# Kernel tuning notes

Measured on AMD Instinct MI355X. Metric: run time of the kernel, lower is better.

## Reference

```python
import jax, jax.numpy as jnp
import numpy as np

B, S, C, H = 8, 1024, 768, 8
D = C // H  # head dim = 96
MLP = 4 * C


def setup_inputs() -> dict:
    key = jax.random.key(0)
    ks = jax.random.split(key, 12)
    sc = 0.02
    return {
        "x": jax.random.normal(ks[0], (B, S, C), jnp.float32),
        "ln1_w": jnp.ones((S, C), jnp.float32),
        "ln1_b": jnp.zeros((S, C), jnp.float32),
        "ln2_w": jnp.ones((S, C), jnp.float32),
        "ln2_b": jnp.zeros((S, C), jnp.float32),
        "qkv_w": jax.random.normal(ks[1], (C, 3 * C), jnp.float32) * sc,
        "proj_w": jax.random.normal(ks[2], (C, C), jnp.float32) * sc,
        "mlp_w1": jax.random.normal(ks[3], (C, MLP), jnp.float32) * sc,
        "mlp_b1": jnp.zeros((MLP,), jnp.float32),
        "mlp_w2": jax.random.normal(ks[4], (MLP, C), jnp.float32) * sc,
        "mlp_b2": jnp.zeros((C,), jnp.float32),
    }


def _layernorm2d(x, w, b, eps=1e-5):
    # normalizes over BOTH (seq, channel) dims, per nn.LayerNorm([length, channel])
    mu = jnp.mean(x, axis=(-2, -1), keepdims=True)
    var = jnp.mean(jnp.square(x - mu), axis=(-2, -1), keepdims=True)
    return (x - mu) * jax.lax.rsqrt(var + eps) * w + b


def _attention(x, qkv_w, proj_w):
    b, s, _ = x.shape
    qkv = (x @ qkv_w).reshape(b, s, 3, H, D)
    q, k, v = qkv[:, :, 0], qkv[:, :, 1], qkv[:, :, 2]  # [b, s, h, d]
    # NOTE: original module applies NO 1/sqrt(d) scaling
    scores = jnp.einsum("bshd,bthd->bhst", q, k)
    attn = jax.nn.softmax(scores, axis=-1)
    out = jnp.einsum("bhst,bthd->bshd", attn, v).reshape(b, s, C)
    return out @ proj_w


def reference(x, ln1_w, ln1_b, ln2_w, ln2_b, qkv_w, proj_w, mlp_w1, mlp_b1, mlp_w2, mlp_b2):
    # dropout is identity in eval mode
    h = x + _attention(_layernorm2d(x, ln1_w, ln1_b), qkv_w, proj_w)
    y = _layernorm2d(h, ln2_w, ln2_b)
    y = jax.nn.gelu(y @ mlp_w1 + mlp_b1, approximate=False)
    return h + (y @ mlp_w2 + mlp_b2)
```

## Files before the change

kernel.cpp:

```cpp
#include <hip/hip_runtime.h>
#include <hip/hip_bf16.h>

#define S_LEN 1024
#define NB 8
#define NC 768
#define NH 8
#define HD 96
#define NMLP 3072
#define SC (S_LEN*NC)
#define BS (NB*S_LEN)

typedef __attribute__((ext_vector_type(8))) unsigned short u16x8;
typedef __attribute__((ext_vector_type(4))) unsigned short u16x4;
typedef __attribute__((ext_vector_type(8))) __bf16 bf16x8;
typedef __attribute__((ext_vector_type(4))) float f32x4;

__device__ __forceinline__ unsigned short f2b(float f) {
  union { __hip_bfloat16 h; unsigned short u; } cvt;
  cvt.h = __float2bfloat16(f);
  return cvt.u;
}

__device__ __forceinline__ void gload16(const unsigned short* g, unsigned short* l) {
  __builtin_amdgcn_global_load_lds(
      (const __attribute__((address_space(1))) unsigned int*)g,
      (__attribute__((address_space(3))) unsigned int*)l, 16, 0, 0);
}

__device__ __forceinline__ float gelu_f(float v) {
  float u = v * (0.7978845608f + 0.0356774081f * v * v);
  float au = fabsf(u);
  float e = __expf(-2.0f * au);
  float th = (1.0f - e) / (1.0f + e);
  th = copysignf(th, u);
  return 0.5f * v * (1.0f + th);
}

template<int EPI>
__global__ __launch_bounds__(512, 1)
void gemm8(const unsigned short* __restrict__ A, int lda,
           const unsigned short* __restrict__ Bt, int ldb,
           void* __restrict__ Cv, int ldc, int K,
           const float* __restrict__ bias,
           const float* __restrict__ residual, int ldr)
{
  __shared__ unsigned short As[3*16384];
  __shared__ unsigned short Bs[3*8192];
  const int tid = threadIdx.x, lane = tid & 63, wid = tid >> 6;
  const int wm = wid & 3, wn = wid >> 2;
  const int r15 = lane & 15, g = lane >> 4;
  const int tm = blockIdx.x * 256, tn = blockIdx.y * 128;
  const int NT = K >> 6;

  const int srow = lane >> 3;
  const int scol = ((lane & 7) ^ srow) << 3;
  const unsigned short* Ag = A  + (size_t)(tm + wid*32 + srow)*lda + scol;
  const unsigned short* Bg = Bt + (size_t)(tn + wid*16 + srow)*ldb + scol;

  const int kx  = (r15 & 7) << 4;
  const int k0b = (g*16) ^ kx;
  const int k1b = (64 + g*16) ^ kx;
  char* AsB = (char*)As;
  char* BsB = (char*)Bs;
  const int arow = (wm*64 + r15) * 128;
  const int brow = (wn*64 + r15) * 128;

#define LDA8(m,ks) (*(const bf16x8*)(AsB + bufA + arow + (m)*2048 + ((ks) ? k1b : k0b)))
#define LDB8(n,ks) (*(const bf16x8*)(BsB + bufB + brow + (n)*2048 + ((ks) ? k1b : k0b)))
#define STGA(i,kk,bf) gload16(Ag + (size_t)((i)*8)*lda + (kk), As + (bf)*16384 + (wid*4 + (i))*512)
#define STGB(i,kk,bf) gload16(Bg + (size_t)((i)*8)*ldb + (kk), Bs + (bf)*8192  + (wid*2 + (i))*512)
#define MFMA16(a8,b8,c) __builtin_amdgcn_mfma_f32_16x16x32_bf16(a8, b8, c, 0, 0, 0)

  f32x4 acc[4][4];
  #pragma unroll
  for (int m = 0; m < 4; ++m)
    #pragma unroll
    for (int n = 0; n < 4; ++n)
      acc[m][n] = (f32x4){0.f, 0.f, 0.f, 0.f};

  STGA(0,0,0); STGA(1,0,0); STGA(2,0,0); STGA(3,0,0); STGB(0,0,0); STGB(1,0,0);
  STGA(0,64,1); STGA(1,64,1); STGA(2,64,1); STGA(3,64,1); STGB(0,64,1); STGB(1,64,1);
  asm volatile("s_waitcnt vmcnt(6)" ::: "memory");
  __builtin_amdgcn_s_barrier();

  int buf = 0, nbuf = 2;
  for (int t = 0; t < NT; ++t) {
    const int kk = (t + 2) << 6;
    const bool pre = (t + 2) < NT;
    const int bufA = buf * 32768;
    const int bufB = buf * 16384;
    bf16x8 a[4][2], b0[2][2], b1[2][2];

    #pragma unroll
    for (int m = 0; m < 4; ++m) { a[m][0] = LDA8(m,0); a[m][1] = LDA8(m,1); }
    #pragma unroll
    for (int n = 0; n < 2; ++n) { b0[n][0] = LDB8(n,0); b0[n][1] = LDB8(n,1); }
    if (pre) { STGA(0,kk,nbuf); STGA(1,kk,nbuf); STGB(0,kk,nbuf); }
    __builtin_amdgcn_s_barrier();
    asm volatile("s_waitcnt lgkmcnt(0)" ::: "memory");
    __builtin_amdgcn_s_setprio(1);
    #pragma unroll
    for (int m = 0; m < 4; ++m)
      #pragma unroll
      for (int n = 0; n < 2; ++n) {
        acc[m][n] = MFMA16(a[m][0], b0[n][0], acc[m][n]);
        acc[m][n] = MFMA16(a[m][1], b0[n][1], acc[m][n]);
      }
    __builtin_amdgcn_s_setprio(0);
    __builtin_amdgcn_s_barrier();

    #pragma unroll
    for (int n = 0; n < 2; ++n) { b1[n][0] = LDB8(n+2,0); b1[n][1] = LDB8(n+2,1); }
    if (pre) { STGA(2,kk,nbuf); STGA(3,kk,nbuf); STGB(1,kk,nbuf); }
    __builtin_amdgcn_s_barrier();
    asm volatile("s_waitcnt lgkmcnt(0)" ::: "memory");
    __builtin_amdgcn_s_setprio(1);
    #pragma unroll
    for (int m = 0; m < 4; ++m)
      #pragma unroll
      for (int n = 0; n < 2; ++n) {
        acc[m][n+2] = MFMA16(a[m][0], b1[n][0], acc[m][n+2]);
        acc[m][n+2] = MFMA16(a[m][1], b1[n][1], acc[m][n+2]);
      }
    __builtin_amdgcn_s_setprio(0);
    if (pre) asm volatile("s_waitcnt vmcnt(6)" ::: "memory");
    else     asm volatile("s_waitcnt vmcnt(0)" ::: "memory");
    __builtin_amdgcn_s_barrier();
    buf  = (buf  == 2) ? 0 : buf  + 1;
    nbuf = (nbuf == 2) ? 0 : nbuf + 1;
  }
#undef LDA8
#undef LDB8
#undef STGA
#undef STGB
#undef MFMA16

  unsigned short* Cu = (unsigned short*)Cv;
  float* Cf = (float*)Cv;
  #pragma unroll
  for (int m = 0; m < 4; ++m) {
    #pragma unroll
    for (int n = 0; n < 4; ++n) {
      const int col = tn + wn*64 + n*16 + r15;
      #pragma unroll
      for (int r = 0; r < 4; ++r) {
        const int row = tm + wm*64 + m*16 + g*4 + r;
        float v = acc[m][n][r];
        if (EPI == 2 || EPI == 4) v += bias[col];
        if (EPI == 3 || EPI == 4) v += residual[(size_t)row*ldr + col];
        if (EPI == 2) v = gelu_f(v);
        if (EPI == 0 || EPI == 2) Cu[(size_t)row*ldc + col] = f2b(v);
        else                      Cf[(size_t)row*ldc + col] = v;
      }
    }
  }
}

__global__ __launch_bounds__(256, 2)
void flash_attn(const unsigned short* __restrict__ qkv,
                const unsigned short* __restrict__ vt,
                unsigned short* __restrict__ outb)
{
  __shared__ unsigned short Ks[128*96];
  __shared__ unsigned short Vs[96*128];
  __shared__ unsigned short Ps[128*128];
  const int tid = threadIdx.x, lane = tid & 63, wq = tid >> 6;
  const int r15 = lane & 15, g = lane >> 4;
  const int bh = blockIdx.y, b = bh >> 3, h = bh & 7;
  const int q0 = blockIdx.x * 128;
  const int swz = (r15 & 7) << 4;
  char* PsB = (char*)Ps;
  char* VsB = (char*)Vs;

  bf16x8 qf[2][3];
  {
    const unsigned short* qb = qkv + ((size_t)b*S_LEN + q0 + wq*32 + r15)*2304 + h*HD + g*8;
    #pragma unroll
    for (int n = 0; n < 2; ++n)
      #pragma unroll
      for (int kc = 0; kc < 3; ++kc)
        qf[n][kc] = *(const bf16x8*)(qb + (size_t)n*16*2304 + kc*32);
  }

  int krow[6], kcol[6], vrow[6], vcol[6];
  #pragma unroll
  for (int i = 0; i < 6; ++i) {
    const int c = (wq*6 + i)*64 + lane;
    krow[i] = c / 12;
    kcol[i] = (c % 12) * 8;
    const int L = c * 16;
    const int row = L >> 8, cb = L & 255;
    vrow[i] = row;
    vcol[i] = (cb ^ ((row & 7) << 4)) >> 1;
  }
  const unsigned short* kbase = qkv + (size_t)b*S_LEN*2304 + NC + h*HD;
  const unsigned short* vbase = vt + (size_t)bh*HD*S_LEN;

  f32x4 oacc[6][2];
  #pragma unroll
  for (int m = 0; m < 6; ++m) {
    oacc[m][0] = (f32x4){0.f,0.f,0.f,0.f};
    oacc[m][1] = (f32x4){0.f,0.f,0.f,0.f};
  }
  float mrun[2] = {-INFINITY, -INFINITY};
  float lrun[2] = {0.f, 0.f};

  for (int kt = 0; kt < 8; ++kt) {
    const unsigned short* ksrc = kbase + (size_t)kt*128*2304;
    const unsigned short* vsrc = vbase + kt*128;
    #pragma unroll
    for (int i = 0; i < 6; ++i) {
      gload16(ksrc + (size_t)krow[i]*2304 + kcol[i], Ks + (wq*6 + i)*512);
      gload16(vsrc + vrow[i]*1024 + vcol[i],         Vs + (wq*6 + i)*512);
    }
    __syncthreads();

    f32x4 sacc[8][2];
    #pragma unroll
    for (int m = 0; m < 8; ++m) {
      sacc[m][0] = (f32x4){0.f,0.f,0.f,0.f};
      sacc[m][1] = (f32x4){0.f,0.f,0.f,0.f};
    }
    __builtin_amdgcn_s_setprio(1);
    #pragma unroll
    for (int kc = 0; kc < 3; ++kc)
      #pragma unroll
      for (int m = 0; m < 8; ++m) {
        bf16x8 kf = *(const bf16x8*)(Ks + (m*16 + r15)*96 + kc*32 + g*8);
        sacc[m][0] = __builtin_amdgcn_mfma_f32_16x16x32_bf16(kf, qf[0][kc], sacc[m][0], 0,0,0);
        sacc[m][1] = __builtin_amdgcn_mfma_f32_16x16x32_bf16(kf, qf[1][kc], sacc[m][1], 0,0,0);
      }
    __builtin_amdgcn_s_setprio(0);

    #pragma unroll
    for (int n = 0; n < 2; ++n) {
      float pm = -INFINITY;
      #pragma unroll
      for (int m = 0; m < 8; ++m)
        #pragma unroll
        for (int r = 0; r < 4; ++r) pm = fmaxf(pm, sacc[m][n][r]);
      pm = fmaxf(pm, __shfl_xor(pm, 16));
      pm = fmaxf(pm, __shfl_xor(pm, 32));
      const float newm = fmaxf(mrun[n], pm);
      const float scale = __expf(mrun[n] - newm);
      mrun[n] = newm;
      const int qloc = wq*32 + n*16 + r15;
      float s = 0.f;
      #pragma unroll
      for (int m = 0; m < 8; ++m) {
        float e0 = __expf(sacc[m][n][0] - newm);
        float e1 = __expf(sacc[m][n][1] - newm);
        float e2 = __expf(sacc[m][n][2] - newm);
        float e3 = __expf(sacc[m][n][3] - newm);
        s += (e0 + e1) + (e2 + e3);
        u16x4 pk = { f2b(e0), f2b(e1), f2b(e2), f2b(e3) };
        *(u16x4*)(PsB + ((qloc*256 + m*32 + g*8) ^ swz)) = pk;
      }
      s += __shfl_xor(s, 16);
      s += __shfl_xor(s, 32);
      lrun[n] = lrun[n]*scale + s;
      #pragma unroll
      for (int m = 0; m < 6; ++m) oacc[m][n] *= scale;
    }

    #pragma unroll
    for (int kc = 0; kc < 4; ++kc) {
      bf16x8 pf0 = *(const bf16x8*)(PsB + (((wq*32      + r15)*256 + kc*64 + g*16) ^ swz));
      bf16x8 pf1 = *(const bf16x8*)(PsB + (((wq*32 + 16 + r15)*256 + kc*64 + g*16) ^ swz));
      __builtin_amdgcn_s_setprio(1);
      #pragma unroll
      for (int m = 0; m < 6; ++m) {
        bf16x8 vf = *(const bf16x8*)(VsB + (((m*16 + r15)*256 + kc*64 + g*16) ^ swz));
        oacc[m][0] = __builtin_amdgcn_mfma_f32_16x16x32_bf16(vf, pf0, oacc[m][0], 0,0,0);
        oacc[m][1] = __builtin_amdgcn_mfma_f32_16x16x32_bf16(vf, pf1, oacc[m][1], 0,0,0);
      }
      __builtin_amdgcn_s_setprio(0);
    }
    __syncthreads();
  }

  #pragma unroll
  for (int n = 0; n < 2; ++n) {
    const float inv = 1.0f / lrun[n];
    unsigned short* orow = outb + ((size_t)b*S_LEN + q0 + wq*32 + n*16 + r15)*NC + h*HD;
    #pragma unroll
    for (int m = 0; m < 6; ++m) {
      u16x4 pk = { f2b(oacc[m][n][0]*inv), f2b(oacc[m][n][1]*inv),
                   f2b(oacc[m][n][2]*inv), f2b(oacc[m][n][3]*inv) };
      *(u16x4*)(orow + m*16 + g*4) = pk;
    }
  }
}

__global__ void transpose_cast(const float* __restrict__ W, unsigned short* __restrict__ Wt,
                               int K, int N)
{
  __shared__ float tile[32][33];
  const int tx = threadIdx.x & 31, ty = threadIdx.x >> 5;
  const int n0 = blockIdx.x * 32, k0 = blockIdx.y * 32;
  #pragma unroll
  for (int i = 0; i < 32; i += 8)
    tile[ty + i][tx] = W[(size_t)(k0 + ty + i)*N + n0 + tx];
  __syncthreads();
  #pragma unroll
  for (int i = 0; i < 32; i += 8)
    Wt[(size_t)(n0 + ty + i)*K + k0 + tx] = f2b(tile[tx][ty + i]);
}

__global__ void transpose_v(const unsigned short* __restrict__ qkv, unsigned short* __restrict__ vt)
{
  __shared__ unsigned short tile[32][33];
  const int bh = blockIdx.z, b = bh >> 3, h = bh & 7;
  const unsigned short* v = qkv + (size_t)b*S_LEN*3*NC + 2*NC + h*HD;
  unsigned short* o = vt + (size_t)bh*HD*S_LEN;
  const int s0 = blockIdx.x * 32, d0 = blockIdx.y * 32;
  const int tx = threadIdx.x & 31, ty = threadIdx.x >> 5;
  #pragma unroll
  for (int i = 0; i < 32; i += 8)
    tile[ty + i][tx] = v[(size_t)(s0 + ty + i)*(3*NC) + d0 + tx];
  __syncthreads();
  #pragma unroll
  for (int i = 0; i < 32; i += 8)
    o[(size_t)(d0 + ty + i)*S_LEN + s0 + tx] = tile[tx][ty + i];
}

__global__ void ln_part(const float* __restrict__ X, float* __restrict__ part)
{
  const int b = blockIdx.x / 96, blk = blockIdx.x % 96;
  const float4* xb = (const float4*)(X + (size_t)b*SC);
  float s = 0.f, s2 = 0.f;
  #pragma unroll
  for (int i = 0; i < 8; ++i) {
    float4 v = xb[blk*2048 + i*256 + threadIdx.x];
    s  += v.x + v.y + v.z + v.w;
    s2 += v.x*v.x + v.y*v.y + v.z*v.z + v.w*v.w;
  }
  #pragma unroll
  for (int o = 32; o; o >>= 1) { s += __shfl_down(s, o); s2 += __shfl_down(s2, o); }
  __shared__ float r1[4], r2[4];
  const int w = threadIdx.x >> 6;
  if ((threadIdx.x & 63) == 0) { r1[w] = s; r2[w] = s2; }
  __syncthreads();
  if (threadIdx.x == 0) {
    part[(b*96 + blk)*2]     = r1[0] + r1[1] + r1[2] + r1[3];
    part[(b*96 + blk)*2 + 1] = r2[0] + r2[1] + r2[2] + r2[3];
  }
}

__global__ void ln_fin(const float* __restrict__ part, float* __restrict__ stats)
{
  const int b = blockIdx.x;
  float s = 0.f, s2 = 0.f;
  for (int i = threadIdx.x; i < 96; i += 64) {
    s  += part[(b*96 + i)*2];
    s2 += part[(b*96 + i)*2 + 1];
  }
  #pragma unroll
  for (int o = 32; o; o >>= 1) { s += __shfl_down(s, o); s2 += __shfl_down(s2, o); }
  if (threadIdx.x == 0) {
    const float inv = 1.0f / (float)SC;
    const float mu = s * inv;
    const float var = s2 * inv - mu*mu;
    stats[b*2] = mu;
    stats[b*2 + 1] = rsqrtf(var + 1e-5f);
  }
}

__global__ void ln_apply(const float* __restrict__ X, const float* __restrict__ W,
                         const float* __restrict__ Bv, const float* __restrict__ stats,
                         unsigned short* __restrict__ out)
{
  const size_t i = ((size_t)blockIdx.x*256 + threadIdx.x) * 8;
  const int b = (int)(i / SC);
  const size_t r = i % SC;
  const float mu = stats[b*2], rs = stats[b*2 + 1];
  float4 x0 = *(const float4*)(X + i),  x1 = *(const float4*)(X + i + 4);
  float4 w0 = *(const float4*)(W + r),  w1 = *(const float4*)(W + r + 4);
  float4 b0 = *(const float4*)(Bv + r), b1 = *(const float4*)(Bv + r + 4);
  u16x8 o;
  o[0] = f2b((x0.x - mu)*rs*w0.x + b0.x);
  o[1] = f2b((x0.y - mu)*rs*w0.y + b0.y);
  o[2] = f2b((x0.z - mu)*rs*w0.z + b0.z);
  o[3] = f2b((x0.w - mu)*rs*w0.w + b0.w);
  o[4] = f2b((x1.x - mu)*rs*w1.x + b1.x);
  o[5] = f2b((x1.y - mu)*rs*w1.y + b1.y);
  o[6] = f2b((x1.z - mu)*rs*w1.z + b1.z);
  o[7] = f2b((x1.w - mu)*rs*w1.w + b1.w);
  *(u16x8*)(out + i) = o;
}

extern "C" void kernel_launch(void* const* d_in, const int* in_sizes, int n_in,
                              void* d_out, int out_size, void* d_ws, size_t ws_size,
                              hipStream_t stream) {
  const float* x      = (const float*)d_in[0];
  const float* ln1_w  = (const float*)d_in[1];
  const float* ln1_b  = (const float*)d_in[2];
  const float* ln2_w  = (const float*)d_in[3];
  const float* ln2_b  = (const float*)d_in[4];
  const float* qkv_w  = (const float*)d_in[5];
  const float* proj_w = (const float*)d_in[6];
  const float* mlp_w1 = (const float*)d_in[7];
  const float* mlp_b1 = (const float*)d_in[8];
  const float* mlp_w2 = (const float*)d_in[9];
  const float* mlp_b2 = (const float*)d_in[10];
  float* out = (float*)d_out;

  char* ws = (char*)d_ws;
  size_t off = 0;
  auto alloc = [&](size_t b) { size_t o = off; off += (b + 255) & ~(size_t)255; return o; };
  unsigned short* wqkvT  = (unsigned short*)(ws + alloc((size_t)3*NC*NC*2));
  unsigned short* wprojT = (unsigned short*)(ws + alloc((size_t)NC*NC*2));
  unsigned short* w1T    = (unsigned short*)(ws + alloc((size_t)NMLP*NC*2));
  unsigned short* w2T    = (unsigned short*)(ws + alloc((size_t)NC*NMLP*2));
  unsigned short* lnbf   = (unsigned short*)(ws + alloc((size_t)BS*NC*2));
  const size_t qkvOff    = alloc((size_t)BS*3*NC*2);
  unsigned short* qkvbf  = (unsigned short*)(ws + qkvOff);
  unsigned short* vt     = (unsigned short*)(ws + alloc((size_t)NB*NH*HD*S_LEN*2));
  unsigned short* ybf    = (unsigned short*)(ws + qkvOff);
  float* hbuf            = (float*)(ws + alloc((size_t)BS*NC*4));
  float* part            = (float*)(ws + alloc((size_t)NB*96*2*4));
  float* stats           = (float*)(ws + alloc((size_t)NB*2*4));
  (void)ws_size; (void)in_sizes; (void)n_in; (void)out_size;

  const dim3 blk(256);
  const dim3 blk512(512);

  transpose_cast<<<dim3(3*NC/32, NC/32),   blk, 0, stream>>>(qkv_w,  wqkvT,  NC, 3*NC);
  transpose_cast<<<dim3(NC/32, NC/32),     blk, 0, stream>>>(proj_w, wprojT, NC, NC);
  transpose_cast<<<dim3(NMLP/32, NC/32),   blk, 0, stream>>>(mlp_w1, w1T,    NC, NMLP);
  transpose_cast<<<dim3(NC/32, NMLP/32),   blk, 0, stream>>>(mlp_w2, w2T,    NMLP, NC);

  ln_part<<<dim3(NB*96), blk, 0, stream>>>(x, part);
  ln_fin<<<dim3(NB), dim3(64), 0, stream>>>(part, stats);
  ln_apply<<<dim3(BS*NC/2048), blk, 0, stream>>>(x, ln1_w, ln1_b, stats, lnbf);

  gemm8<0><<<dim3(BS/256, 3*NC/128), blk512, 0, stream>>>(
      lnbf, NC, wqkvT, NC, qkvbf, 3*NC, NC, nullptr, nullptr, 0);

  transpose_v<<<dim3(S_LEN/32, HD/32, NB*NH), blk, 0, stream>>>(qkvbf, vt);

  flash_attn<<<dim3(S_LEN/128, NB*NH), blk, 0, stream>>>(qkvbf, vt, lnbf);

  gemm8<3><<<dim3(BS/256, NC/128), blk512, 0, stream>>>(
      lnbf, NC, wprojT, NC, hbuf, NC, NC, nullptr, x, NC);

  ln_part<<<dim3(NB*96), blk, 0, stream>>>(hbuf, part);
  ln_fin<<<dim3(NB), dim3(64), 0, stream>>>(part, stats);
  ln_apply<<<dim3(BS*NC/2048), blk, 0, stream>>>(hbuf, ln2_w, ln2_b, stats, lnbf);

  gemm8<2><<<dim3(BS/256, NMLP/128), blk512, 0, stream>>>(
      lnbf, NC, w1T, NC, ybf, NMLP, NC, mlp_b1, nullptr, 0);

  gemm8<4><<<dim3(BS/256, NC/128), blk512, 0, stream>>>(
      ybf, NMLP, w2T, NMLP, out, NC, NMLP, mlp_b2, hbuf, NC);
}
```

Before: 283.6 us.

## Fuse LN2 statistics into proj GEMM epilogue and add 256x256 MLP1 GEMM

The projection GEMM epilogue now accumulates per-batch sum and sum-of-squares and adds them atomically into a small buffer. This removes the separate ln_part/ln_fin passes over hbuf, and a new ln_apply_f computes mean and variance from those sums. A new 256x256-tile GEMM with double-buffered LDS replaces the 256x128 kernel for the MLP up-projection to raise data reuse per block. The single-pass E[x^2]-mu^2 variance in fp32 risks cancellation error. The atomics also make the statistics order-dependent from run to run.

```diff
diff --git a/kernel.cpp b/kernel.cpp
--- a/kernel.cpp
+++ b/kernel.cpp
@@ -38,11 +38,152 @@
 
 template<int EPI>
 __global__ __launch_bounds__(512, 1)
+void gemm256(const unsigned short* __restrict__ A, int lda,
+             const unsigned short* __restrict__ Bt, int ldb,
+             void* __restrict__ Cv, int ldc, int K,
+             const float* __restrict__ bias,
+             const float* __restrict__ residual, int ldr)
+{
+  __shared__ unsigned short As[4*8192];
+  __shared__ unsigned short Bs[4*8192];
+  const int tid = threadIdx.x, lane = tid & 63, wid = tid >> 6;
+  const int wm = wid & 1, wn = wid >> 1;
+  const int r15 = lane & 15, g = lane >> 4;
+  const int tm = blockIdx.x * 256, tn = blockIdx.y * 256;
+  const int NT = K >> 6;
+
+  const int srow = lane >> 3;
+  const int schunk = ((lane & 7) ^ srow) << 3;
+  const unsigned short* Ag = A  + (size_t)(tm + wid*16 + srow)*lda + schunk;
+  const unsigned short* Bg = Bt + (size_t)(tn + wid*16 + srow)*ldb + schunk;
+
+  const int c0 = ((g)     ^ (r15 & 7)) << 4;
+  const int c1 = ((4 | g) ^ (r15 & 7)) << 4;
+  char* AsB = (char*)As;
+  char* BsB = (char*)Bs;
+
+#define STGA(h,i,kk,sl) gload16(Ag + (size_t)((h)*128 + (i)*8)*lda + (kk), As + (sl)*8192 + (wid*16 + (i)*8)*64)
+#define STGB(h,i,kk,sl) gload16(Bg + (size_t)((h)*128 + (i)*8)*ldb + (kk), Bs + (sl)*8192 + (wid*16 + (i)*8)*64)
+#define LDA8(fm,cb,sl) (*(const bf16x8*)(AsB + (sl)*16384 + ((fm)*16 + r15)*128 + (cb)))
+#define LDB8(n,cb,sl)  (*(const bf16x8*)(BsB + (sl)*16384 + ((wn&1)*64 + (n)*16 + r15)*128 + (cb)))
+#define MFMA(a8,b8,c) __builtin_amdgcn_mfma_f32_16x16x32_bf16(a8, b8, c, 0, 0, 0)
+
+  f32x4 acc[8][4];
+  #pragma unroll
+  for (int m = 0; m < 8; ++m)
+    #pragma unroll
+    for (int n = 0; n < 4; ++n)
+      acc[m][n] = (f32x4){0.f, 0.f, 0.f, 0.f};
+
+  STGA(0,0,0,0); STGA(0,1,0,0); STGA(1,0,0,1); STGA(1,1,0,1);
+  STGB(0,0,0,0); STGB(0,1,0,0); STGB(1,0,0,1); STGB(1,1,0,1);
+  asm volatile("s_waitcnt vmcnt(0)" ::: "memory");
+  __builtin_amdgcn_s_barrier();
+
+  for (int kt = 0; kt < NT; ++kt) {
+    const int rd = (kt & 1) * 2, wr = rd ^ 2;
+    const int kk = (kt + 1) << 6;
+    const bool pre = (kt + 1) < NT;
+    const int asl = rd + wm;
+    const int bsl = rd + (wn >> 1);
+    bf16x8 a[4], b[4];
+
+    #pragma unroll
+    for (int m = 0; m < 4; ++m) a[m] = LDA8(m, c0, asl);
+    #pragma unroll
+    for (int n = 0; n < 4; ++n) b[n] = LDB8(n, c0, bsl);
+    if (pre) { STGA(0,0,kk,wr); STGA(0,1,kk,wr); }
+    __builtin_amdgcn_s_barrier();
+    asm volatile("s_waitcnt lgkmcnt(0)" ::: "memory");
+    __builtin_amdgcn_s_setprio(1);
+    #pragma unroll
+    for (int m = 0; m < 4; ++m)
+      #pragma unroll
+      for (int n = 0; n < 4; ++n)
+        acc[m][n] = MFMA(a[m], b[n], acc[m][n]);
+    __builtin_amdgcn_s_setprio(0);
+    __builtin_amdgcn_s_barrier();
+
+    #pragma unroll
+    for (int m = 0; m < 4; ++m) a[m] = LDA8(m + 4, c0, asl);
+    if (pre) { STGA(1,0,kk,wr+1); STGA(1,1,kk,wr+1); }
+    __builtin_amdgcn_s_barrier();
+    asm volatile("s_waitcnt lgkmcnt(0)" ::: "memory");
+    __builtin_amdgcn_s_setprio(1);
+    #pragma unroll
+    for (int m = 0; m < 4; ++m)
+      #pragma unroll
+      for (int n = 0; n < 4; ++n)
+        acc[m + 4][n] = MFMA(a[m], b[n], acc[m + 4][n]);
+    __builtin_amdgcn_s_setprio(0);
+    __builtin_amdgcn_s_barrier();
+
+    #pragma unroll
+    for (int m = 0; m < 4; ++m) a[m] = LDA8(m, c1, asl);
+    #pragma unroll
+    for (int n = 0; n < 4; ++n) b[n] = LDB8(n, c1, bsl);
+    if (pre) { STGB(0,0,kk,wr); STGB(0,1,kk,wr); }
+    __builtin_amdgcn_s_barrier();
+    asm volatile("s_waitcnt lgkmcnt(0)" ::: "memory");
+    __builtin_amdgcn_s_setprio(1);
+    #pragma unroll
+    for (int m = 0; m < 4; ++m)
+      #pragma unroll
+      for (int n = 0; n < 4; ++n)
+        acc[m][n] = MFMA(a[m], b[n], acc[m][n]);
+    __builtin_amdgcn_s_setprio(0);
+    __builtin_amdgcn_s_barrier();
+
+    #pragma unroll
+    for (int m = 0; m < 4; ++m) a[m] = LDA8(m + 4, c1, asl);
+    if (pre) { STGB(1,0,kk,wr+1); STGB(1,1,kk,wr+1); }
+    __builtin_amdgcn_s_barrier();
+    asm volatile("s_waitcnt lgkmcnt(0)" ::: "memory");
+    __builtin_amdgcn_s_setprio(1);
+    #pragma unroll
+    for (int m = 0; m < 4; ++m)
+      #pragma unroll
+      for (int n = 0; n < 4; ++n)
+        acc[m + 4][n] = MFMA(a[m], b[n], acc[m + 4][n]);
+    __builtin_amdgcn_s_setprio(0);
+    asm volatile("s_waitcnt vmcnt(0)" ::: "memory");
+    __builtin_amdgcn_s_barrier();
+  }
+#undef STGA
+#undef STGB
+#undef LDA8
+#undef LDB8
+#undef MFMA
+
+  unsigned short* Cu = (unsigned short*)Cv;
+  float* Cf = (float*)Cv;
+  #pragma unroll
+  for (int m = 0; m < 8; ++m) {
+    #pragma unroll
+    for (int n = 0; n < 4; ++n) {
+      const int col = tn + wn*64 + n*16 + r15;
+      #pragma unroll
+      for (int r = 0; r < 4; ++r) {
+        const int row = tm + wm*128 + m*16 + g*4 + r;
+        float v = acc[m][n][r];
+        if (EPI == 2 || EPI == 4) v += bias[col];
+        if (EPI == 3 || EPI == 4) v += residual[(size_t)row*ldr + col];
+        if (EPI == 2) v = gelu_f(v);
+        if (EPI == 0 || EPI == 2) Cu[(size_t)row*ldc + col] = f2b(v);
+        else                      Cf[(size_t)row*ldc + col] = v;
+      }
+    }
+  }
+}
+
+template<int EPI>
+__global__ __launch_bounds__(512, 1)
 void gemm8(const unsigned short* __restrict__ A, int lda,
            const unsigned short* __restrict__ Bt, int ldb,
            void* __restrict__ Cv, int ldc, int K,
            const float* __restrict__ bias,
-           const float* __restrict__ residual, int ldr)
+           const float* __restrict__ residual, int ldr,
+           float* __restrict__ lnred)
 {
   __shared__ unsigned short As[3*16384];
   __shared__ unsigned short Bs[3*8192];
@@ -137,6 +278,7 @@
 
   unsigned short* Cu = (unsigned short*)Cv;
   float* Cf = (float*)Cv;
+  float s1 = 0.f, s2 = 0.f;
   #pragma unroll
   for (int m = 0; m < 4; ++m) {
     #pragma unroll
@@ -149,9 +291,26 @@
         if (EPI == 2 || EPI == 4) v += bias[col];
         if (EPI == 3 || EPI == 4) v += residual[(size_t)row*ldr + col];
         if (EPI == 2) v = gelu_f(v);
+        if (EPI == 3) { s1 += v; s2 += v*v; }
         if (EPI == 0 || EPI == 2) Cu[(size_t)row*ldc + col] = f2b(v);
         else                      Cf[(size_t)row*ldc + col] = v;
       }
+    }
+  }
+  if (EPI == 3) {
+    #pragma unroll
+    for (int o = 32; o; o >>= 1) { s1 += __shfl_xor(s1, o); s2 += __shfl_xor(s2, o); }
+    __syncthreads();
+    float* red = (float*)As;
+    if (lane == 0) { red[wid*2] = s1; red[wid*2+1] = s2; }
+    __syncthreads();
+    if (tid == 0) {
+      float a1 = 0.f, a2 = 0.f;
+      #pragma unroll
+      for (int w = 0; w < 8; ++w) { a1 += red[w*2]; a2 += red[w*2+1]; }
+      const int bidx = tm >> 10;
+      atomicAdd(&lnred[bidx*2],     a1);
+      atomicAdd(&lnred[bidx*2 + 1], a2);
     }
   }
 }
@@ -389,6 +548,32 @@
   *(u16x8*)(out + i) = o;
 }
 
+__global__ void ln_apply_f(const float* __restrict__ X, const float* __restrict__ W,
+                           const float* __restrict__ Bv, const float* __restrict__ red,
+                           unsigned short* __restrict__ out)
+{
+  const size_t i = ((size_t)blockIdx.x*256 + threadIdx.x) * 8;
+  const int b = (int)(i / SC);
+  const size_t r = i % SC;
+  const float inv = 1.0f / (float)SC;
+  const float mu = red[b*2] * inv;
+  const float var = red[b*2 + 1] * inv - mu*mu;
+  const float rs = rsqrtf(var + 1e-5f);
+  float4 x0 = *(const float4*)(X + i),  x1 = *(const float4*)(X + i + 4);
+  float4 w0 = *(const float4*)(W + r),  w1 = *(const float4*)(W + r + 4);
+  float4 b0 = *(const float4*)(Bv + r), b1 = *(const float4*)(Bv + r + 4);
+  u16x8 o;
+  o[0] = f2b((x0.x - mu)*rs*w0.x + b0.x);
+  o[1] = f2b((x0.y - mu)*rs*w0.y + b0.y);
+  o[2] = f2b((x0.z - mu)*rs*w0.z + b0.z);
+  o[3] = f2b((x0.w - mu)*rs*w0.w + b0.w);
+  o[4] = f2b((x1.x - mu)*rs*w1.x + b1.x);
+  o[5] = f2b((x1.y - mu)*rs*w1.y + b1.y);
+  o[6] = f2b((x1.z - mu)*rs*w1.z + b1.z);
+  o[7] = f2b((x1.w - mu)*rs*w1.w + b1.w);
+  *(u16x8*)(out + i) = o;
+}
+
 extern "C" void kernel_launch(void* const* d_in, const int* in_sizes, int n_in,
                               void* d_out, int out_size, void* d_ws, size_t ws_size,
                               hipStream_t stream) {
@@ -420,10 +605,13 @@
   float* hbuf            = (float*)(ws + alloc((size_t)BS*NC*4));
   float* part            = (float*)(ws + alloc((size_t)NB*96*2*4));
   float* stats           = (float*)(ws + alloc((size_t)NB*2*4));
+  float* lnred           = (float*)(ws + alloc((size_t)NB*2*4));
   (void)ws_size; (void)in_sizes; (void)n_in; (void)out_size;
 
   const dim3 blk(256);
   const dim3 blk512(512);
+
+  hipMemsetAsync(lnred, 0, NB*2*sizeof(float), stream);
 
   transpose_cast<<<dim3(3*NC/32, NC/32),   blk, 0, stream>>>(qkv_w,  wqkvT,  NC, 3*NC);
   transpose_cast<<<dim3(NC/32, NC/32),     blk, 0, stream>>>(proj_w, wprojT, NC, NC);
@@ -435,22 +623,20 @@
   ln_apply<<<dim3(BS*NC/2048), blk, 0, stream>>>(x, ln1_w, ln1_b, stats, lnbf);
 
   gemm8<0><<<dim3(BS/256, 3*NC/128), blk512, 0, stream>>>(
-      lnbf, NC, wqkvT, NC, qkvbf, 3*NC, NC, nullptr, nullptr, 0);
+      lnbf, NC, wqkvT, NC, qkvbf, 3*NC, NC, nullptr, nullptr, 0, nullptr);
 
   transpose_v<<<dim3(S_LEN/32, HD/32, NB*NH), blk, 0, stream>>>(qkvbf, vt);
 
   flash_attn<<<dim3(S_LEN/128, NB*NH), blk, 0, stream>>>(qkvbf, vt, lnbf);
 
   gemm8<3><<<dim3(BS/256, NC/128), blk512, 0, stream>>>(
-      lnbf, NC, wprojT, NC, hbuf, NC, NC, nullptr, x, NC);
-
-  ln_part<<<dim3(NB*96), blk, 0, stream>>>(hbuf, part);
-  ln_fin<<<dim3(NB), dim3(64), 0, stream>>>(part, stats);
-  ln_apply<<<dim3(BS*NC/2048), blk, 0, stream>>>(hbuf, ln2_w, ln2_b, stats, lnbf);
-
-  gemm8<2><<<dim3(BS/256, NMLP/128), blk512, 0, stream>>>(
+      lnbf, NC, wprojT, NC, hbuf, NC, NC, nullptr, x, NC, lnred);
+
+  ln_apply_f<<<dim3(BS*NC/2048), blk, 0, stream>>>(hbuf, ln2_w, ln2_b, lnred, lnbf);
+
+  gemm256<2><<<dim3(BS/256, NMLP/256), blk512, 0, stream>>>(
       lnbf, NC, w1T, NC, ybf, NMLP, NC, mlp_b1, nullptr, 0);
 
   gemm8<4><<<dim3(BS/256, NC/128), blk512, 0, stream>>>(
-      ybf, NMLP, w2T, NMLP, out, NC, NMLP, mlp_b2, hbuf, NC);
-}
+      ybf, NMLP, w2T, NMLP, out, NC, NMLP, mlp_b2, hbuf, NC, nullptr);
+}
```

New measurement: 293.5 us. 3.5% more time.

## Fuse LN2 statistics into proj GEMM epilogue via atomics; add sched barriers

Applied to the files above, without the earlier changes.

The projection GEMM epilogue now accumulates per-batch sum and sum-of-squares of the residual output and atomically adds them into a small buffer. A new ln_apply_f derives mean and variance from those sums, which removes the separate ln_part and ln_fin passes over hbuf. Scheduling barriers are also placed around the s_barrier/waitcnt points of the GEMM main loop to stop the compiler from reordering across them. The single-pass E[x²]-mu² variance is less numerically robust than the two-pass version, and float atomics make the sums nondeterministic.

```diff
diff --git a/kernel.cpp b/kernel.cpp
--- a/kernel.cpp
+++ b/kernel.cpp
@@ -42,7 +42,8 @@
            const unsigned short* __restrict__ Bt, int ldb,
            void* __restrict__ Cv, int ldc, int K,
            const float* __restrict__ bias,
-           const float* __restrict__ residual, int ldr)
+           const float* __restrict__ residual, int ldr,
+           float* __restrict__ lnred)
 {
   __shared__ unsigned short As[3*16384];
   __shared__ unsigned short Bs[3*8192];
@@ -70,6 +71,7 @@
 #define STGA(i,kk,bf) gload16(Ag + (size_t)((i)*8)*lda + (kk), As + (bf)*16384 + (wid*4 + (i))*512)
 #define STGB(i,kk,bf) gload16(Bg + (size_t)((i)*8)*ldb + (kk), Bs + (bf)*8192  + (wid*2 + (i))*512)
 #define MFMA16(a8,b8,c) __builtin_amdgcn_mfma_f32_16x16x32_bf16(a8, b8, c, 0, 0, 0)
+#define SBAR() __builtin_amdgcn_sched_barrier(0)
 
   f32x4 acc[4][4];
   #pragma unroll
@@ -96,8 +98,10 @@
     #pragma unroll
     for (int n = 0; n < 2; ++n) { b0[n][0] = LDB8(n,0); b0[n][1] = LDB8(n,1); }
     if (pre) { STGA(0,kk,nbuf); STGA(1,kk,nbuf); STGB(0,kk,nbuf); }
+    SBAR();
     __builtin_amdgcn_s_barrier();
     asm volatile("s_waitcnt lgkmcnt(0)" ::: "memory");
+    SBAR();
     __builtin_amdgcn_s_setprio(1);
     #pragma unroll
     for (int m = 0; m < 4; ++m)
@@ -107,13 +111,16 @@
         acc[m][n] = MFMA16(a[m][1], b0[n][1], acc[m][n]);
       }
     __builtin_amdgcn_s_setprio(0);
+    SBAR();
     __builtin_amdgcn_s_barrier();
 
     #pragma unroll
     for (int n = 0; n < 2; ++n) { b1[n][0] = LDB8(n+2,0); b1[n][1] = LDB8(n+2,1); }
     if (pre) { STGA(2,kk,nbuf); STGA(3,kk,nbuf); STGB(1,kk,nbuf); }
+    SBAR();
     __builtin_amdgcn_s_barrier();
     asm volatile("s_waitcnt lgkmcnt(0)" ::: "memory");
+    SBAR();
     __builtin_amdgcn_s_setprio(1);
     #pragma unroll
     for (int m = 0; m < 4; ++m)
@@ -123,6 +130,7 @@
         acc[m][n+2] = MFMA16(a[m][1], b1[n][1], acc[m][n+2]);
       }
     __builtin_amdgcn_s_setprio(0);
+    SBAR();
     if (pre) asm volatile("s_waitcnt vmcnt(6)" ::: "memory");
     else     asm volatile("s_waitcnt vmcnt(0)" ::: "memory");
     __builtin_amdgcn_s_barrier();
@@ -134,9 +142,11 @@
 #undef STGA
 #undef STGB
 #undef MFMA16
+#undef SBAR
 
   unsigned short* Cu = (unsigned short*)Cv;
   float* Cf = (float*)Cv;
+  float s1 = 0.f, s2 = 0.f;
   #pragma unroll
   for (int m = 0; m < 4; ++m) {
     #pragma unroll
@@ -149,9 +159,26 @@
         if (EPI == 2 || EPI == 4) v += bias[col];
         if (EPI == 3 || EPI == 4) v += residual[(size_t)row*ldr + col];
         if (EPI == 2) v = gelu_f(v);
+        if (EPI == 3) { s1 += v; s2 += v*v; }
         if (EPI == 0 || EPI == 2) Cu[(size_t)row*ldc + col] = f2b(v);
         else                      Cf[(size_t)row*ldc + col] = v;
       }
+    }
+  }
+  if (EPI == 3) {
+    #pragma unroll
+    for (int o = 32; o; o >>= 1) { s1 += __shfl_xor(s1, o); s2 += __shfl_xor(s2, o); }
+    __syncthreads();
+    float* red = (float*)As;
+    if (lane == 0) { red[wid*2] = s1; red[wid*2+1] = s2; }
+    __syncthreads();
+    if (tid == 0) {
+      float a1 = 0.f, a2 = 0.f;
+      #pragma unroll
+      for (int w = 0; w < 8; ++w) { a1 += red[w*2]; a2 += red[w*2+1]; }
+      const int bidx = tm >> 10;
+      atomicAdd(&lnred[bidx*2],     a1);
+      atomicAdd(&lnred[bidx*2 + 1], a2);
     }
   }
 }
@@ -389,6 +416,32 @@
   *(u16x8*)(out + i) = o;
 }
 
+__global__ void ln_apply_f(const float* __restrict__ X, const float* __restrict__ W,
+                           const float* __restrict__ Bv, const float* __restrict__ red,
+                           unsigned short* __restrict__ out)
+{
+  const size_t i = ((size_t)blockIdx.x*256 + threadIdx.x) * 8;
+  const int b = (int)(i / SC);
+  const size_t r = i % SC;
+  const float inv = 1.0f / (float)SC;
+  const float mu = red[b*2] * inv;
+  const float var = red[b*2 + 1] * inv - mu*mu;
+  const float rs = rsqrtf(var + 1e-5f);
+  float4 x0 = *(const float4*)(X + i),  x1 = *(const float4*)(X + i + 4);
+  float4 w0 = *(const float4*)(W + r),  w1 = *(const float4*)(W + r + 4);
+  float4 b0 = *(const float4*)(Bv + r), b1 = *(const float4*)(Bv + r + 4);
+  u16x8 o;
+  o[0] = f2b((x0.x - mu)*rs*w0.x + b0.x);
+  o[1] = f2b((x0.y - mu)*rs*w0.y + b0.y);
+  o[2] = f2b((x0.z - mu)*rs*w0.z + b0.z);
+  o[3] = f2b((x0.w - mu)*rs*w0.w + b0.w);
+  o[4] = f2b((x1.x - mu)*rs*w1.x + b1.x);
+  o[5] = f2b((x1.y - mu)*rs*w1.y + b1.y);
+  o[6] = f2b((x1.z - mu)*rs*w1.z + b1.z);
+  o[7] = f2b((x1.w - mu)*rs*w1.w + b1.w);
+  *(u16x8*)(out + i) = o;
+}
+
 extern "C" void kernel_launch(void* const* d_in, const int* in_sizes, int n_in,
                               void* d_out, int out_size, void* d_ws, size_t ws_size,
                               hipStream_t stream) {
@@ -420,10 +473,13 @@
   float* hbuf            = (float*)(ws + alloc((size_t)BS*NC*4));
   float* part            = (float*)(ws + alloc((size_t)NB*96*2*4));
   float* stats           = (float*)(ws + alloc((size_t)NB*2*4));
+  float* lnred           = (float*)(ws + alloc((size_t)NB*2*4));
   (void)ws_size; (void)in_sizes; (void)n_in; (void)out_size;
 
   const dim3 blk(256);
   const dim3 blk512(512);
+
+  hipMemsetAsync(lnred, 0, NB*2*sizeof(float), stream);
 
   transpose_cast<<<dim3(3*NC/32, NC/32),   blk, 0, stream>>>(qkv_w,  wqkvT,  NC, 3*NC);
   transpose_cast<<<dim3(NC/32, NC/32),     blk, 0, stream>>>(proj_w, wprojT, NC, NC);
@@ -435,22 +491,20 @@
   ln_apply<<<dim3(BS*NC/2048), blk, 0, stream>>>(x, ln1_w, ln1_b, stats, lnbf);
 
   gemm8<0><<<dim3(BS/256, 3*NC/128), blk512, 0, stream>>>(
-      lnbf, NC, wqkvT, NC, qkvbf, 3*NC, NC, nullptr, nullptr, 0);
+      lnbf, NC, wqkvT, NC, qkvbf, 3*NC, NC, nullptr, nullptr, 0, nullptr);
 
   transpose_v<<<dim3(S_LEN/32, HD/32, NB*NH), blk, 0, stream>>>(qkvbf, vt);
 
   flash_attn<<<dim3(S_LEN/128, NB*NH), blk, 0, stream>>>(qkvbf, vt, lnbf);
 
   gemm8<3><<<dim3(BS/256, NC/128), blk512, 0, stream>>>(
-      lnbf, NC, wprojT, NC, hbuf, NC, NC, nullptr, x, NC);
-
-  ln_part<<<dim3(NB*96), blk, 0, stream>>>(hbuf, part);
-  ln_fin<<<dim3(NB), dim3(64), 0, stream>>>(part, stats);
-  ln_apply<<<dim3(BS*NC/2048), blk, 0, stream>>>(hbuf, ln2_w, ln2_b, stats, lnbf);
+      lnbf, NC, wprojT, NC, hbuf, NC, NC, nullptr, x, NC, lnred);
+
+  ln_apply_f<<<dim3(BS*NC/2048), blk, 0, stream>>>(hbuf, ln2_w, ln2_b, lnred, lnbf);
 
   gemm8<2><<<dim3(BS/256, NMLP/128), blk512, 0, stream>>>(
-      lnbf, NC, w1T, NC, ybf, NMLP, NC, mlp_b1, nullptr, 0);
+      lnbf, NC, w1T, NC, ybf, NMLP, NC, mlp_b1, nullptr, 0, nullptr);
 
   gemm8<4><<<dim3(BS/256, NC/128), blk512, 0, stream>>>(
-      ybf, NMLP, w2T, NMLP, out, NC, NMLP, mlp_b2, hbuf, NC);
-}
+      ybf, NMLP, w2T, NMLP, out, NC, NMLP, mlp_b2, hbuf, NC, nullptr);
+}
```

Result: no change. 284.9 us (+0.5%).
